# Optimization experiments

Hardware: AMD Instinct MI355X
Metric: run time of the kernel (lower is better)

## Reference

```python
import jax, jax.numpy as jnp
import numpy as np

INNER_DIM = 1024

def setup_inputs() -> dict:
    key = jax.random.key(0)
    ks = jax.random.split(key, 6)
    b, n, d = 4, 4096, 1024
    s = 0.02
    return {
        "x": jax.random.normal(ks[0], (b, n, d), jnp.float32),
        "y": jax.random.normal(ks[1], (b, n, d), jnp.float32),
        "Wq": jax.random.normal(ks[2], (INNER_DIM, d), jnp.float32) * s,
        "Wk": jax.random.normal(ks[3], (INNER_DIM, d), jnp.float32) * s,
        "Wv": jax.random.normal(ks[4], (INNER_DIM, d), jnp.float32) * s,
        "Wo": jax.random.normal(ks[5], (d, INNER_DIM), jnp.float32) * s,
        "bo": jnp.zeros((d,), jnp.float32),
    }

def reference(x, y, Wq, Wk, Wv, Wo, bo):
    # torch Linear: out = inp @ W.T ; weights stored [out_dim, in_dim]
    q = jnp.einsum('bnd,ed->bne', y, Wq)  # queries come from y
    k = jnp.einsum('bnd,ed->bne', x, Wk)
    v = jnp.einsum('bnd,ed->bne', x, Wv)
    dk = 1.0 / jnp.sqrt(jnp.asarray(INNER_DIM, q.dtype))  # full inner_dim, not per-head
    alpha = jnp.einsum('bie,bje->bij', q, k) * dk  # [b, n, n] full score matrix
    alpha = jax.nn.softmax(alpha, axis=-1)
    # NOTE: original masked_fill is a no-op (result discarded), so no causal mask.
    ctx = jnp.einsum('bij,bje->bie', alpha, v)
    return jnp.einsum('bie,de->bid', ctx, Wo) + bo
```

## Files before the change

### kernel.cpp

```cpp
#include <hip/hip_runtime.h>
#include <stdint.h>

typedef __attribute__((ext_vector_type(8))) short s16x8;
typedef __attribute__((ext_vector_type(4))) float f32x4;

__device__ __forceinline__ unsigned short f2bf(float f) {
    union { float f; uint32_t u; } c; c.f = f;
    uint32_t u = c.u + 0x7FFFu + ((c.u >> 16) & 1u);
    return (unsigned short)(u >> 16);
}

__device__ __forceinline__ float bf2f(unsigned int u16) {
    union { uint32_t u; float f; } c; c.u = u16 << 16;
    return c.f;
}

__device__ __forceinline__ void load_lds16(const unsigned short* g, unsigned short* l) {
    __builtin_amdgcn_global_load_lds(
        (const __attribute__((address_space(1))) char*)(uintptr_t)g,
        (__attribute__((address_space(3))) char*)(uint32_t)(uintptr_t)l,
        16, 0, 0);
}

__device__ __forceinline__ void gemm256_core(
    const unsigned short* __restrict__ Ap, long lda,
    const unsigned short* __restrict__ Bp, long ldb,
    int nt, unsigned short* As, unsigned short* Bs, f32x4 (*acc)[4])
{
    const int tid  = threadIdx.x;
    const int wv   = tid >> 6;
    const int lane = tid & 63;
    const int cl   = lane & 15;
    const int qd   = lane >> 4;
    const int wm   = wv >> 2;
    const int wn   = wv & 3;

    long srcA[2][2], srcB[2][2];
    int  dstL[2][2];
#pragma unroll
    for (int h = 0; h < 2; ++h)
#pragma unroll
        for (int c = 0; c < 2; ++c) {
            const int q0    = (wv << 7) + (c << 6);
            const int phys0 = q0 + (q0 & 512) + (h << 9);
            const int phys  = phys0 + lane;
            const int g     = phys >> 3;
            const long koff = (long)(((lane & 7) ^ (g & 7)) << 3);
            srcA[h][c] = (long)g * lda + koff;
            srcB[h][c] = (long)g * ldb + koff;
            dstL[h][c] = phys0 << 3;
        }

    const int k0off = (((qd    ) ^ (cl & 7)) << 3) + cl * 64;
    const int k1off = (((4 + qd) ^ (cl & 7)) << 3) + cl * 64;
    const int aB = wm << 3;
    const int bB = wn << 2;

#define STAGE_A(buf, kb, h) do {                                             \
        load_lds16(Ap + (kb) + srcA[h][0], As + ((buf) << 14) + dstL[h][0]); \
        load_lds16(Ap + (kb) + srcA[h][1], As + ((buf) << 14) + dstL[h][1]); \
    } while (0)
#define STAGE_B(buf, kb, h) do {                                             \
        load_lds16(Bp + (kb) + srcB[h][0], Bs + ((buf) << 14) + dstL[h][0]); \
        load_lds16(Bp + (kb) + srcB[h][1], Bs + ((buf) << 14) + dstL[h][1]); \
    } while (0)
#define VMW(n) asm volatile("s_waitcnt vmcnt(" #n ")" ::: "memory")
#define BAR()  asm volatile("s_barrier" ::: "memory")

    STAGE_B(0, 0, 0); STAGE_B(0, 0, 1); STAGE_A(0, 0, 0); STAGE_A(0, 0, 1);
    STAGE_B(1, 64, 0); STAGE_B(1, 64, 1); STAGE_A(1, 64, 0);
    VMW(8);
    BAR();

    s16x8 bfr[4][2];

#define PHASE(AB, BB, Q, RB, STG, WT) do {                                   \
        const unsigned short* Ab_ = As + ((AB) << 14);                       \
        const unsigned short* Bb_ = Bs + ((BB) << 14);                       \
        s16x8 af_[2][2];                                                     \
        _Pragma("unroll")                                                    \
        for (int i_ = 0; i_ < 2; ++i_) {                                     \
            const int s_ = aB + (Q) * 2 + i_;                                \
            af_[i_][0] = *(const s16x8*)&Ab_[s_ * 1024 + k0off];             \
            af_[i_][1] = *(const s16x8*)&Ab_[s_ * 1024 + k1off];             \
        }                                                                    \
        if (RB) {                                                            \
            _Pragma("unroll")                                                \
            for (int j_ = 0; j_ < 4; ++j_) {                                 \
                const int s_ = bB + j_;                                      \
                bfr[j_][0] = *(const s16x8*)&Bb_[s_ * 1024 + k0off];         \
                bfr[j_][1] = *(const s16x8*)&Bb_[s_ * 1024 + k1off];         \
            }                                                                \
        }                                                                    \
        STG;                                                                 \
        WT;                                                                  \
        BAR();                                                               \
        __builtin_amdgcn_s_setprio(1);                                       \
        _Pragma("unroll")                                                    \
        for (int i_ = 0; i_ < 2; ++i_)                                       \
            _Pragma("unroll")                                                \
            for (int j_ = 0; j_ < 4; ++j_) {                                 \
                acc[(Q) * 2 + i_][j_] =                                      \
                    __builtin_amdgcn_mfma_f32_16x16x32_bf16(                 \
                        af_[i_][0], bfr[j_][0], acc[(Q) * 2 + i_][j_],       \
                        0, 0, 0);                                            \
                acc[(Q) * 2 + i_][j_] =                                      \
                    __builtin_amdgcn_mfma_f32_16x16x32_bf16(                 \
                        af_[i_][1], bfr[j_][1], acc[(Q) * 2 + i_][j_],       \
                        0, 0, 0);                                            \
            }                                                                \
        __builtin_amdgcn_s_setprio(0);                                       \
        BAR();                                                               \
    } while (0)

    const int ni = nt >> 1;
#pragma unroll 1
    for (int it = 0; it < ni; ++it) {
        const bool more = (it + 1) < ni;
        const long kb_o  = ((long)(2 * it + 1)) << 6;
        const long kb_e2 = ((long)(2 * it + 2)) << 6;
        const long kb_o2 = ((long)(2 * it + 3)) << 6;

        PHASE(0, 0, 0, true,  STAGE_A(1, kb_o, 1), (void)0);
        PHASE(0, 0, 1, false, if (more) STAGE_B(0, kb_e2, 0),
              if (more) VMW(10); else VMW(8));
        PHASE(0, 0, 2, false, if (more) STAGE_B(0, kb_e2, 1), (void)0);
        PHASE(0, 0, 3, false, if (more) STAGE_A(0, kb_e2, 0),
              if (more) VMW(8); else VMW(2));
        PHASE(1, 1, 0, true,  if (more) STAGE_A(0, kb_e2, 1), (void)0);
        PHASE(1, 1, 1, false, if (more) STAGE_B(1, kb_o2, 0),
              if (more) VMW(10); else VMW(0));
        PHASE(1, 1, 2, false, if (more) STAGE_B(1, kb_o2, 1), (void)0);
        PHASE(1, 1, 3, false, if (more) STAGE_A(1, kb_o2, 0),
              if (more) VMW(8));
    }
#undef PHASE
#undef STAGE_A
#undef STAGE_B
#undef VMW
#undef BAR
}

template <bool OUT_BF16, bool HAS_BIAS, bool EXP_OUT>
__global__ __launch_bounds__(512, 2)
void gemm256(const unsigned short* __restrict__ A, long lda, long sA,
             const unsigned short* __restrict__ B, long ldb, long sB,
             void* __restrict__ C, long ldc, long sC,
             const float* __restrict__ bias, int K, float scale)
{
    __shared__ __align__(16) unsigned short As[2 * 16384];
    __shared__ __align__(16) unsigned short Bs[2 * 16384];

    const unsigned gx = gridDim.x, gy = gridDim.y;
    const unsigned lin = blockIdx.x + gx * blockIdx.y;
    unsigned bxs, bys;
    if ((gy & 7u) == 0u) {
        const unsigned g = lin & 7u, j = lin >> 3;
        bxs = j & (gx - 1u);
        bys = g * (gy >> 3) + j / gx;
    } else { bxs = blockIdx.x; bys = blockIdx.y; }

    const unsigned short* Ap = A + (long)blockIdx.z * sA + (long)bys * 256 * lda;
    const unsigned short* Bp = B + (long)blockIdx.z * sB + (long)bxs * 256 * ldb;

    f32x4 acc[8][4];
#pragma unroll
    for (int i = 0; i < 8; ++i)
#pragma unroll
        for (int j = 0; j < 4; ++j)
            acc[i][j] = f32x4{0.f, 0.f, 0.f, 0.f};

    gemm256_core(Ap, lda, Bp, ldb, K >> 6, As, Bs, acc);

    const int wv = threadIdx.x >> 6;
    const int wm = wv >> 2, wn = wv & 3;
    const int cl = threadIdx.x & 15, qd = (threadIdx.x & 63) >> 4;
    const long row0 = (long)bys * 256 + wm * 128;
    const long col0 = (long)bxs * 256 + wn * 64;
    const long zC   = (long)blockIdx.z * sC;
#pragma unroll
    for (int j = 0; j < 4; ++j) {
        const long c = col0 + j * 16 + cl;
        float badd = 0.f;
        if constexpr (HAS_BIAS) badd = bias[c];
#pragma unroll
        for (int i = 0; i < 8; ++i) {
            const long rb = row0 + i * 16 + qd * 4;
#pragma unroll
            for (int r = 0; r < 4; ++r) {
                float v = acc[i][j][r] * scale + badd;
                if constexpr (EXP_OUT) v = __expf(v);
                const long idx = zC + (rb + r) * ldc + c;
                if constexpr (OUT_BF16) ((unsigned short*)C)[idx] = f2bf(v);
                else                    ((float*)C)[idx] = v;
            }
        }
    }
}

__global__ __launch_bounds__(512, 2)
void gemm256_pv4(const unsigned short* __restrict__ p0,
                 const unsigned short* __restrict__ p1,
                 const unsigned short* __restrict__ p2,
                 const unsigned short* __restrict__ p3,
                 const unsigned short* __restrict__ Bv, long ldb, long sB,
                 unsigned short* __restrict__ C, long ldc, long sC,
                 const float* __restrict__ rowdiv, int K, long lda)
{
    __shared__ __align__(16) unsigned short As[2 * 16384];
    __shared__ __align__(16) unsigned short Bs[2 * 16384];

    const unsigned gx = gridDim.x, gy = gridDim.y;
    const unsigned lin = blockIdx.x + gx * blockIdx.y;
    unsigned bxs, bys;
    if ((gy & 7u) == 0u) {
        const unsigned g = lin & 7u, j = lin >> 3;
        bxs = j & (gx - 1u);
        bys = g * (gy >> 3) + j / gx;
    } else { bxs = blockIdx.x; bys = blockIdx.y; }

    const int z = blockIdx.z;
    const unsigned short* A = (z == 0) ? p0 : (z == 1) ? p1 : (z == 2) ? p2 : p3;

    const unsigned short* Ap = A + (long)bys * 256 * lda;
    const unsigned short* Bp = Bv + (long)z * sB + (long)bxs * 256 * ldb;

    f32x4 acc[8][4];
#pragma unroll
    for (int i = 0; i < 8; ++i)
#pragma unroll
        for (int j = 0; j < 4; ++j)
            acc[i][j] = f32x4{0.f, 0.f, 0.f, 0.f};

    gemm256_core(Ap, lda, Bp, ldb, K >> 6, As, Bs, acc);

    const int wv = threadIdx.x >> 6;
    const int wm = wv >> 2, wn = wv & 3;
    const int cl = threadIdx.x & 15, qd = (threadIdx.x & 63) >> 4;
    const long row0 = (long)bys * 256 + wm * 128;
    const long col0 = (long)bxs * 256 + wn * 64;
    const long zC   = (long)z * sC;
    const float* rd = rowdiv + (long)z * 4096;
#pragma unroll
    for (int i = 0; i < 8; ++i) {
        const long rb = row0 + i * 16 + qd * 4;
        float rinv[4];
#pragma unroll
        for (int r = 0; r < 4; ++r) rinv[r] = 1.f / rd[rb + r];
#pragma unroll
        for (int j = 0; j < 4; ++j) {
            const long c = col0 + j * 16 + cl;
#pragma unroll
            for (int r = 0; r < 4; ++r)
                C[zC + (rb + r) * ldc + c] = f2bf(acc[i][j][r] * rinv[r]);
        }
    }
}

__global__ __launch_bounds__(256)
void rowsum4(const unsigned short* __restrict__ p0,
             const unsigned short* __restrict__ p1,
             const unsigned short* __restrict__ p2,
             const unsigned short* __restrict__ p3,
             float* __restrict__ rs)
{
    const unsigned row = blockIdx.x;
    const unsigned b = row >> 12;
    const unsigned short* P = (b == 0) ? p0 : (b == 1) ? p1 : (b == 2) ? p2 : p3;
    const long r = row & 4095u;
    const int tid = threadIdx.x, lane = tid & 63, wave = tid >> 6;

    const uint4* src = (const uint4*)(P + r * 4096);
    uint4 u0 = src[tid], u1 = src[tid + 256];
    float s = 0.f;
    {
        const unsigned* a = (const unsigned*)&u0;
        const unsigned* c = (const unsigned*)&u1;
#pragma unroll
        for (int i = 0; i < 4; ++i) {
            s += bf2f(a[i] & 0xFFFFu) + bf2f(a[i] >> 16);
            s += bf2f(c[i] & 0xFFFFu) + bf2f(c[i] >> 16);
        }
    }
#pragma unroll
    for (int off = 32; off > 0; off >>= 1) s += __shfl_xor(s, off);
    __shared__ float red[4];
    if (lane == 0) red[wave] = s;
    __syncthreads();
    if (tid == 0) rs[row] = red[0] + red[1] + red[2] + red[3];
}

__global__ __launch_bounds__(256)
void cast2_bf16(const float* __restrict__ s0, unsigned short* __restrict__ d0,
                const float* __restrict__ s1, unsigned short* __restrict__ d1)
{
    const float*    in  = blockIdx.y ? s1 : s0;
    unsigned short* out = blockIdx.y ? d1 : d0;
    const long i = ((long)blockIdx.x * 256 + threadIdx.x) * 4;
    const float4 v = *(const float4*)(in + i);
    ushort4 o;
    o.x = f2bf(v.x); o.y = f2bf(v.y); o.z = f2bf(v.z); o.w = f2bf(v.w);
    *(ushort4*)(out + i) = o;
}

__global__ __launch_bounds__(256)
void cast4_bf16(const float* __restrict__ s0, unsigned short* __restrict__ d0,
                const float* __restrict__ s1, unsigned short* __restrict__ d1,
                const float* __restrict__ s2, unsigned short* __restrict__ d2,
                const float* __restrict__ s3, unsigned short* __restrict__ d3)
{
    const float* in; unsigned short* out;
    switch (blockIdx.y) {
        case 0: in = s0; out = d0; break;
        case 1: in = s1; out = d1; break;
        case 2: in = s2; out = d2; break;
        default: in = s3; out = d3; break;
    }
    const long i = ((long)blockIdx.x * 256 + threadIdx.x) * 4;
    const float4 v = *(const float4*)(in + i);
    ushort4 o;
    o.x = f2bf(v.x); o.y = f2bf(v.y); o.z = f2bf(v.z); o.w = f2bf(v.w);
    *(ushort4*)(out + i) = o;
}

extern "C" void kernel_launch(void* const* d_in, const int* in_sizes, int n_in,
                              void* d_out, int out_size, void* d_ws, size_t ws_size,
                              hipStream_t stream)
{
    (void)in_sizes; (void)n_in; (void)out_size;
    const float* x  = (const float*)d_in[0];
    const float* y  = (const float*)d_in[1];
    const float* Wq = (const float*)d_in[2];
    const float* Wk = (const float*)d_in[3];
    const float* Wv = (const float*)d_in[4];
    const float* Wo = (const float*)d_in[5];
    const float* bo = (const float*)d_in[6];
    float* out = (float*)d_out;

    const long N = 4096, D = 1024;
    const long NB = N * D;
    const size_t MiB = 1ull << 20;
    const float dk = 0.03125f;
    char* w = (char*)d_ws;

    if (ws_size >= 200 * MiB) {
        unsigned short* Xb  = (unsigned short*)(w);
        unsigned short* Yb  = (unsigned short*)(w + 32 * MiB);
        unsigned short* Qb  = (unsigned short*)(w + 64 * MiB);
        unsigned short* Kb  = (unsigned short*)(w + 96 * MiB);
        unsigned short* VT  = (unsigned short*)(w + 128 * MiB);
        unsigned short* Wqb = (unsigned short*)(w + 192 * MiB);
        unsigned short* Wkb = (unsigned short*)(w + 194 * MiB);
        unsigned short* Wvb = (unsigned short*)(w + 196 * MiB);
        unsigned short* Wob = (unsigned short*)(w + 198 * MiB);
        unsigned short* P0  = (unsigned short*)(w);
        unsigned short* P1  = (unsigned short*)(w + 32 * MiB);
        unsigned short* P2  = (unsigned short*)(w + 160 * MiB);
        unsigned short* P3  = (unsigned short*)d_out;
        unsigned short* Cx  = (unsigned short*)(w + 64 * MiB);
        float*          rsm = (float*)(w + 192 * MiB);

        cast2_bf16<<<dim3(16384, 2), dim3(256), 0, stream>>>(x, Xb, y, Yb);
        cast4_bf16<<<dim3(1024, 4),  dim3(256), 0, stream>>>(
            Wq, Wqb, Wk, Wkb, Wv, Wvb, Wo, Wob);

        gemm256<true, false, false><<<dim3(4, 64, 2), dim3(512), 0, stream>>>(
            Yb, D, (long)(Xb - Yb), Wqb, D, (long)(Wkb - Wqb),
            Qb, D, (long)(Kb - Qb), nullptr, (int)D, 1.f);
        gemm256<true, false, false><<<dim3(16, 4, 4), dim3(512), 0, stream>>>(
            Wvb, D, 0, Xb, D, NB, VT, N, NB, nullptr, (int)D, 1.f);

        gemm256<true, false, true><<<dim3(16, 16, 2), dim3(512), 0, stream>>>(
            Qb, D, NB, Kb, D, NB, P0, N, (long)(P1 - P0), nullptr, (int)D, dk);
        gemm256<true, false, true><<<dim3(16, 16, 2), dim3(512), 0, stream>>>(
            Qb + 2 * NB, D, NB, Kb + 2 * NB, D, NB,
            P2, N, (long)(P3 - P2), nullptr, (int)D, dk);
        rowsum4<<<dim3(16384), dim3(256), 0, stream>>>(P0, P1, P2, P3, rsm);

        gemm256_pv4<<<dim3(4, 16, 4), dim3(512), 0, stream>>>(
            P0, P1, P2, P3, VT, N, NB, Cx, D, NB, rsm, (int)N, N);
        gemm256<false, true, false><<<dim3(4, 64, 1), dim3(512), 0, stream>>>(
            Cx, D, 0, Wob, D, 0, out, D, 0, bo, (int)D, 1.f);
    } else if (ws_size >= 104 * MiB) {
        unsigned short* Wqb = (unsigned short*)(w);
        unsigned short* Wkb = (unsigned short*)(w + 2 * MiB);
        unsigned short* Wvb = (unsigned short*)(w + 4 * MiB);
        unsigned short* Wob = (unsigned short*)(w + 6 * MiB);
        unsigned short* xb  = (unsigned short*)(w + 8 * MiB);
        unsigned short* yb  = (unsigned short*)(w + 16 * MiB);
        unsigned short* Qb  = (unsigned short*)(w + 24 * MiB);
        unsigned short* Kb  = (unsigned short*)(w + 32 * MiB);
        unsigned short* VTb = (unsigned short*)(w + 40 * MiB);
        unsigned short* Cxb = (unsigned short*)(w + 48 * MiB);
        unsigned short* Pb  = (unsigned short*)(w + 56 * MiB);
        float*          rsm = (float*)(w + 88 * MiB);

        cast4_bf16<<<dim3(1024, 4), dim3(256), 0, stream>>>(
            Wq, Wqb, Wk, Wkb, Wv, Wvb, Wo, Wob);

        for (int b = 0; b < 4; ++b) {
            cast2_bf16<<<dim3(4096, 2), dim3(256), 0, stream>>>(
                x + b * NB, xb, y + b * NB, yb);
            gemm256<true, false, false><<<dim3(4, 16, 1), dim3(512), 0, stream>>>(
                yb, D, 0, Wqb, D, 0, Qb, D, 0, nullptr, (int)D, 1.f);
            gemm256<true, false, false><<<dim3(4, 16, 1), dim3(512), 0, stream>>>(
                xb, D, 0, Wkb, D, 0, Kb, D, 0, nullptr, (int)D, 1.f);
            gemm256<true, false, false><<<dim3(16, 4, 1), dim3(512), 0, stream>>>(
                Wvb, D, 0, xb, D, 0, VTb, N, 0, nullptr, (int)D, 1.f);
            gemm256<true, false, true><<<dim3(16, 16, 1), dim3(512), 0, stream>>>(
                Qb, D, 0, Kb, D, 0, Pb, N, 0, nullptr, (int)D, dk);
            rowsum4<<<dim3(4096), dim3(256), 0, stream>>>(Pb, Pb, Pb, Pb, rsm);
            gemm256_pv4<<<dim3(4, 16, 1), dim3(512), 0, stream>>>(
                Pb, Pb, Pb, Pb, VTb, N, 0, Cxb, D, 0, rsm, (int)N, N);
            gemm256<false, true, false><<<dim3(4, 16, 1), dim3(512), 0, stream>>>(
                Cxb, D, 0, Wob, D, 0, out + b * NB, D, 0, bo, (int)D, 1.f);
        }
    }
}
```

Measured before the change: 644.6 us.

## Software-pipeline LDS fragment reads one phase ahead of MFMAs in GEMM core

Restructures the 256x256 GEMM main loop so A-fragment LDS reads for the next phase are issued before the current phase's MFMAs, using two register sets. This halves the barriers per phase and overlaps LDS latency with matrix math. It also merges the A/B source offset arrays, assuming lda equals ldb, which silently breaks if the strides differ. Register pressure rises, and the wait-count bookkeeping is hand-tuned, so any mismatch risks a race.

```diff
diff --git a/kernel.cpp b/kernel.cpp
--- a/kernel.cpp
+++ b/kernel.cpp
@@ -27,6 +27,7 @@
     const unsigned short* __restrict__ Bp, long ldb,
     int nt, unsigned short* As, unsigned short* Bs, f32x4 (*acc)[4])
 {
+    (void)ldb;
     const int tid  = threadIdx.x;
     const int wv   = tid >> 6;
     const int lane = tid & 63;
@@ -35,7 +36,7 @@
     const int wm   = wv >> 2;
     const int wn   = wv & 3;
 
-    long srcA[2][2], srcB[2][2];
+    long src[2][2];
     int  dstL[2][2];
 #pragma unroll
     for (int h = 0; h < 2; ++h)
@@ -46,8 +47,7 @@
             const int phys  = phys0 + lane;
             const int g     = phys >> 3;
             const long koff = (long)(((lane & 7) ^ (g & 7)) << 3);
-            srcA[h][c] = (long)g * lda + koff;
-            srcB[h][c] = (long)g * ldb + koff;
+            src[h][c]  = (long)g * lda + koff;
             dstL[h][c] = phys0 << 3;
         }
 
@@ -57,61 +57,55 @@
     const int bB = wn << 2;
 
 #define STAGE_A(buf, kb, h) do {                                             \
-        load_lds16(Ap + (kb) + srcA[h][0], As + ((buf) << 14) + dstL[h][0]); \
-        load_lds16(Ap + (kb) + srcA[h][1], As + ((buf) << 14) + dstL[h][1]); \
+        load_lds16(Ap + (kb) + src[h][0], As + ((buf) << 14) + dstL[h][0]);  \
+        load_lds16(Ap + (kb) + src[h][1], As + ((buf) << 14) + dstL[h][1]);  \
     } while (0)
 #define STAGE_B(buf, kb, h) do {                                             \
-        load_lds16(Bp + (kb) + srcB[h][0], Bs + ((buf) << 14) + dstL[h][0]); \
-        load_lds16(Bp + (kb) + srcB[h][1], Bs + ((buf) << 14) + dstL[h][1]); \
+        load_lds16(Bp + (kb) + src[h][0], Bs + ((buf) << 14) + dstL[h][0]);  \
+        load_lds16(Bp + (kb) + src[h][1], Bs + ((buf) << 14) + dstL[h][1]);  \
     } while (0)
 #define VMW(n) asm volatile("s_waitcnt vmcnt(" #n ")" ::: "memory")
+#define VMLG(n) asm volatile("s_waitcnt vmcnt(" #n ") lgkmcnt(0)" ::: "memory")
 #define BAR()  asm volatile("s_barrier" ::: "memory")
-
-    STAGE_B(0, 0, 0); STAGE_B(0, 0, 1); STAGE_A(0, 0, 0); STAGE_A(0, 0, 1);
-    STAGE_B(1, 64, 0); STAGE_B(1, 64, 1); STAGE_A(1, 64, 0);
-    VMW(8);
-    BAR();
-
-    s16x8 bfr[4][2];
-
-#define PHASE(AB, BB, Q, RB, STG, WT) do {                                   \
-        const unsigned short* Ab_ = As + ((AB) << 14);                       \
-        const unsigned short* Bb_ = Bs + ((BB) << 14);                       \
-        s16x8 af_[2][2];                                                     \
+#define READ_AF(DST, AB, S0) do {                                            \
         _Pragma("unroll")                                                    \
         for (int i_ = 0; i_ < 2; ++i_) {                                     \
-            const int s_ = aB + (Q) * 2 + i_;                                \
-            af_[i_][0] = *(const s16x8*)&Ab_[s_ * 1024 + k0off];             \
-            af_[i_][1] = *(const s16x8*)&Ab_[s_ * 1024 + k1off];             \
+            const int s_ = aB + (S0) + i_;                                   \
+            DST[i_][0] = *(const s16x8*)&As[((AB) << 14) + s_ * 1024 + k0off];\
+            DST[i_][1] = *(const s16x8*)&As[((AB) << 14) + s_ * 1024 + k1off];\
         }                                                                    \
-        if (RB) {                                                            \
-            _Pragma("unroll")                                                \
-            for (int j_ = 0; j_ < 4; ++j_) {                                 \
-                const int s_ = bB + j_;                                      \
-                bfr[j_][0] = *(const s16x8*)&Bb_[s_ * 1024 + k0off];         \
-                bfr[j_][1] = *(const s16x8*)&Bb_[s_ * 1024 + k1off];         \
-            }                                                                \
+    } while (0)
+#define READ_BF(BB) do {                                                     \
+        _Pragma("unroll")                                                    \
+        for (int j_ = 0; j_ < 4; ++j_) {                                     \
+            const int s_ = bB + j_;                                          \
+            bfr[j_][0] = *(const s16x8*)&Bs[((BB) << 14) + s_ * 1024 + k0off];\
+            bfr[j_][1] = *(const s16x8*)&Bs[((BB) << 14) + s_ * 1024 + k1off];\
         }                                                                    \
-        STG;                                                                 \
-        WT;                                                                  \
-        BAR();                                                               \
+    } while (0)
+#define MFMA16(B0, AF) do {                                                  \
         __builtin_amdgcn_s_setprio(1);                                       \
         _Pragma("unroll")                                                    \
         for (int i_ = 0; i_ < 2; ++i_)                                       \
             _Pragma("unroll")                                                \
             for (int j_ = 0; j_ < 4; ++j_) {                                 \
-                acc[(Q) * 2 + i_][j_] =                                      \
+                acc[(B0) + i_][j_] =                                         \
                     __builtin_amdgcn_mfma_f32_16x16x32_bf16(                 \
-                        af_[i_][0], bfr[j_][0], acc[(Q) * 2 + i_][j_],       \
-                        0, 0, 0);                                            \
-                acc[(Q) * 2 + i_][j_] =                                      \
+                        AF[i_][0], bfr[j_][0], acc[(B0) + i_][j_], 0, 0, 0); \
+                acc[(B0) + i_][j_] =                                         \
                     __builtin_amdgcn_mfma_f32_16x16x32_bf16(                 \
-                        af_[i_][1], bfr[j_][1], acc[(Q) * 2 + i_][j_],       \
-                        0, 0, 0);                                            \
+                        AF[i_][1], bfr[j_][1], acc[(B0) + i_][j_], 0, 0, 0); \
             }                                                                \
         __builtin_amdgcn_s_setprio(0);                                       \
-        BAR();                                                               \
     } while (0)
+
+    STAGE_B(0, 0, 0); STAGE_B(0, 0, 1); STAGE_A(0, 0, 0); STAGE_A(0, 0, 1);
+    STAGE_B(1, 64, 0); STAGE_B(1, 64, 1); STAGE_A(1, 64, 0);
+    VMW(8);
+    BAR();
+
+    s16x8 bfr[4][2], afX[2][2], afY[2][2];
+    READ_AF(afX, 0, 0);
 
     const int ni = nt >> 1;
 #pragma unroll 1
@@ -121,24 +115,49 @@
         const long kb_e2 = ((long)(2 * it + 2)) << 6;
         const long kb_o2 = ((long)(2 * it + 3)) << 6;
 
-        PHASE(0, 0, 0, true,  STAGE_A(1, kb_o, 1), (void)0);
-        PHASE(0, 0, 1, false, if (more) STAGE_B(0, kb_e2, 0),
-              if (more) VMW(10); else VMW(8));
-        PHASE(0, 0, 2, false, if (more) STAGE_B(0, kb_e2, 1), (void)0);
-        PHASE(0, 0, 3, false, if (more) STAGE_A(0, kb_e2, 0),
-              if (more) VMW(8); else VMW(2));
-        PHASE(1, 1, 0, true,  if (more) STAGE_A(0, kb_e2, 1), (void)0);
-        PHASE(1, 1, 1, false, if (more) STAGE_B(1, kb_o2, 0),
-              if (more) VMW(10); else VMW(0));
-        PHASE(1, 1, 2, false, if (more) STAGE_B(1, kb_o2, 1), (void)0);
-        PHASE(1, 1, 3, false, if (more) STAGE_A(1, kb_o2, 0),
-              if (more) VMW(8));
-    }
-#undef PHASE
+        READ_BF(0);
+        READ_AF(afY, 0, 2);
+        STAGE_A(1, kb_o, 1);
+        VMLG(8);
+        BAR();
+        MFMA16(0, afX);
+        READ_AF(afX, 0, 4);
+        if (more) STAGE_B(0, kb_e2, 0);
+        BAR();
+        MFMA16(2, afY);
+        READ_AF(afY, 0, 6);
+        if (more) { STAGE_B(0, kb_e2, 1); VMW(6); } else VMW(2);
+        BAR();
+        MFMA16(4, afX);
+        READ_AF(afX, 1, 0);
+        if (more) STAGE_A(0, kb_e2, 0);
+        BAR();
+        MFMA16(6, afY);
+        READ_BF(1);
+        READ_AF(afY, 1, 2);
+        if (more) { STAGE_A(0, kb_e2, 1); VMLG(8); } else VMLG(0);
+        BAR();
+        MFMA16(0, afX);
+        READ_AF(afX, 1, 4);
+        if (more) STAGE_B(1, kb_o2, 0);
+        BAR();
+        MFMA16(2, afY);
+        READ_AF(afY, 1, 6);
+        if (more) { STAGE_B(1, kb_o2, 1); VMW(6); }
+        BAR();
+        MFMA16(4, afX);
+        if (more) { READ_AF(afX, 0, 0); STAGE_A(1, kb_o2, 0); }
+        BAR();
+        MFMA16(6, afY);
+    }
 #undef STAGE_A
 #undef STAGE_B
 #undef VMW
+#undef VMLG
 #undef BAR
+#undef READ_AF
+#undef READ_BF
+#undef MFMA16
 }
 
 template <bool OUT_BF16, bool HAS_BIAS, bool EXP_OUT>
```

New measurement: 619.8 us. -3.9%, faster.
